# Optimization experiments

Hardware: AMD Instinct MI355X
Metric: run time of the kernel (lower is better)

Reference implementation:

```python
import jax, jax.numpy as jnp
import numpy as np

D, DH, NH = 256, 32, 8  # d_model, d_head, n_heads


def conv2d(x, w, stride=1, padding='VALID', groups=1):
    return jax.lax.conv_general_dilated(
        x, w, (stride, stride), padding,
        feature_group_count=groups,
        dimension_numbers=('NCHW', 'OIHW', 'NCHW'))


def bn2d(x, p):
    # p: [4, C] rows = gamma, beta, running_mean, running_var (inference-mode BN)
    g, b, m, v = p[0], p[1], p[2], p[3]
    inv = g / jnp.sqrt(v + 1e-5)
    return (x - m[:, None, None]) * inv[:, None, None] + b[:, None, None]


def gelu(x):
    return jax.nn.gelu(x, approximate=False)  # torch nn.GELU default (erf)


def to_heads(x):
    # [b, heads*d, h, w] -> [b, h*w, heads, d]
    b, c, h, w = x.shape
    return x.reshape(b, NH, DH, h * w).transpose(0, 3, 1, 2)


def from_heads(x, h, w):
    # [b, h*w, heads, d] -> [b, heads*d, h, w]
    b = x.shape[0]
    return x.transpose(0, 2, 3, 1).reshape(b, NH * DH, h, w)


def linear_attention(q, k, v, eps=1e-6):
    # LoFTR linear attention: phi(x) = elu(x) + 1
    Q = jax.nn.elu(q) + 1.0
    K = jax.nn.elu(k) + 1.0
    L = v.shape[1]
    vn = v / L
    KV = jnp.einsum('nshd,nshv->nhdv', K, vn)
    Z = 1.0 / (jnp.einsum('nlhd,nhd->nlh', Q, K.sum(axis=1)) + eps)
    return jnp.einsum('nlhd,nhdv,nlh->nlhv', Q, KV, Z) * L


def upsample_bilinear_ac(x, s):
    # bilinear, align_corners=True, integer scale factor s (separable H then W)
    def interp(a, axis):
        n_in = a.shape[axis]
        n_out = n_in * s
        pos = jnp.arange(n_out) * ((n_in - 1) / (n_out - 1))
        i0 = jnp.floor(pos).astype(jnp.int32)
        i1 = jnp.minimum(i0 + 1, n_in - 1)
        t = (pos - i0.astype(pos.dtype)).astype(a.dtype)
        sh = [1] * a.ndim
        sh[axis] = n_out
        t = t.reshape(sh)
        return jnp.take(a, i0, axis=axis) * (1 - t) + jnp.take(a, i1, axis=axis) * t
    return interp(interp(x, 2), 3)


def _bn_params(key, c):
    k1, k2, k3, k4 = jax.random.split(key, 4)
    return jnp.stack([
        1.0 + 0.05 * jax.random.normal(k1, (c,)),
        0.05 * jax.random.normal(k2, (c,)),
        0.05 * jax.random.normal(k3, (c,)),
        0.5 + jax.random.uniform(k4, (c,))]).astype(jnp.float32)


def setup_inputs() -> dict:
    key = jax.random.key(0)
    ks = jax.random.split(key, 24)
    B, H, W = 4, 128, 128
    Dm = 4 * D  # MB hidden dim (mlp_ratio=4)

    def w(k, shape, fan_in):
        return (jax.random.normal(k, shape) / np.sqrt(fan_in)).astype(jnp.float32)

    return {
        'x0': jax.random.normal(ks[0], (B, D, H, W), dtype=jnp.float32),
        'scale_weight': jnp.ones((3,), jnp.float32),
        'bn_pre': _bn_params(ks[1], D),
        'wq1': w(ks[2], (D, D, 1, 1), D),
        'wk1': w(ks[3], (D, D, 1, 1), D),
        'wv1': w(ks[4], (D, D, 1, 1), D),
        'wq2': w(ks[5], (D, D, 2, 2), D * 4),
        'wk2': w(ks[6], (D, D, 2, 2), D * 4),
        'wv2': w(ks[7], (D, D, 2, 2), D * 4),
        'wq3': w(ks[8], (D, D, 4, 4), D * 16),
        'wk3': w(ks[9], (D, D, 4, 4), D * 16),
        'wv3': w(ks[10], (D, D, 4, 4), D * 16),
        'merge_w': w(ks[11], (D, D, 1, 1), D),
        'merge_b': 0.01 * jax.random.normal(ks[12], (D,), dtype=jnp.float32),
        'mb_w1': w(ks[13], (Dm, D, 1, 1), D),
        'bn_mb1': _bn_params(ks[14], Dm),
        'mb_wdw': w(ks[15], (Dm, 1, 3, 3), 9),
        'bn_mb2': _bn_params(ks[16], Dm),
        'mb_w2': w(ks[17], (D, Dm, 1, 1), Dm),
        'bn_mb3': _bn_params(ks[18], D),
    }


def reference(x0, scale_weight, bn_pre, wq1, wk1, wv1, wq2, wk2, wv2,
              wq3, wk3, wv3, merge_w, merge_b, mb_w1, bn_mb1, mb_wdw,
              bn_mb2, mb_w2, bn_mb3):
    b, d, h, w = x0.shape
    xn = gelu(bn2d(x0, bn_pre))  # x1 is None -> x1 = x0, shared pre_normact
    # multi-scale conv QKV projections (strides 1, 2, 4)
    q1 = to_heads(conv2d(xn, wq1)); k1 = to_heads(conv2d(xn, wk1)); v1 = to_heads(conv2d(xn, wv1))
    q2 = to_heads(conv2d(xn, wq2, 2)); k2 = to_heads(conv2d(xn, wk2, 2)); v2 = to_heads(conv2d(xn, wv2, 2))
    q3 = to_heads(conv2d(xn, wq3, 4)); k3 = to_heads(conv2d(xn, wk3, 4)); v3 = to_heads(conv2d(xn, wv3, 4))
    o1 = from_heads(linear_attention(q1, k1, v1), h, w)
    o2 = from_heads(linear_attention(q2, k2, v2), h // 2, w // 2)
    o3 = from_heads(linear_attention(q3, k3, v3), h // 4, w // 4)
    o2 = upsample_bilinear_ac(o2, 2)
    o3 = upsample_bilinear_ac(o3, 4)
    sw = jax.nn.softmax(scale_weight)
    message = sw[0] * o1 + sw[1] * o2 + sw[2] * o3
    x = x0 + conv2d(message, merge_w) + merge_b[:, None, None]  # DropPath(0) = id
    # MB mlp: 1x1 expand -> BN -> GELU -> 3x3 depthwise -> BN -> GELU -> 1x1 -> BN
    hm = gelu(bn2d(conv2d(x, mb_w1), bn_mb1))
    hm = gelu(bn2d(conv2d(hm, mb_wdw, 1, ((1, 1), (1, 1)), groups=mb_wdw.shape[0]), bn_mb2))
    mlp_out = bn2d(conv2d(hm, mb_w2), bn_mb3)
    return x + mlp_out
```

## Files before the change

### kernel.cpp

```cpp
#include <hip/hip_runtime.h>
#include <hip/hip_bf16.h>

typedef __attribute__((ext_vector_type(4))) float f32x4;
typedef __attribute__((ext_vector_type(8))) short short8;
typedef unsigned int u32;
typedef unsigned short u16;

__device__ __forceinline__ float bf2f(u16 x) { return __uint_as_float(((u32)x) << 16); }
__device__ __forceinline__ u16 f2bf(float f) {
  u32 u = __float_as_uint(f);
  return (u16)((u + 0x7fffu + ((u >> 16) & 1u)) >> 16);
}
__device__ __forceinline__ float gelu_f(float x) { return 0.5f * x * (1.f + erff(x * 0.7071067811865475f)); }
__device__ __forceinline__ float phi_f(float x) { return x > 0.f ? x + 1.f : __expf(x); }
__device__ __forceinline__ void load8f(const __hip_bfloat16* p, float* f) {
  ushort4 a = *(const ushort4*)p, b = *(const ushort4*)(p + 4);
  f[0] = bf2f(a.x); f[1] = bf2f(a.y); f[2] = bf2f(a.z); f[3] = bf2f(a.w);
  f[4] = bf2f(b.x); f[5] = bf2f(b.y); f[6] = bf2f(b.z); f[7] = bf2f(b.w);
}
__device__ __forceinline__ void cvt8(uint4 u, float* f) {
  f[0] = bf2f((u16)(u.x & 0xffff)); f[1] = bf2f((u16)(u.x >> 16));
  f[2] = bf2f((u16)(u.y & 0xffff)); f[3] = bf2f((u16)(u.y >> 16));
  f[4] = bf2f((u16)(u.z & 0xffff)); f[5] = bf2f((u16)(u.z >> 16));
  f[6] = bf2f((u16)(u.w & 0xffff)); f[7] = bf2f((u16)(u.w >> 16));
}
__device__ __forceinline__ void gload16(const void* g, void* l) {
  __builtin_amdgcn_global_load_lds((const __attribute__((address_space(1))) u32*)g,
                                   (__attribute__((address_space(3))) u32*)l, 16, 0, 0);
}

static constexpr size_t MiB = 1048576ull;
static constexpr size_t OFF_BNP_S = 0, OFF_BNP_T = 1024;
static constexpr size_t OFF_BN1_S = 2048, OFF_BN1_T = 6144;
static constexpr size_t OFF_BN2_S = 10240, OFF_BN2_T = 14336;
static constexpr size_t OFF_BN3_S = 18432, OFF_BN3_T = 19456;
static constexpr size_t OFF_WDW   = 20480;
static constexpr size_t OFF_KV    = 57344;
static constexpr size_t OFF_KSUM  = 450560;
static constexpr size_t OFF_W     = 524288;
static constexpr size_t WF1 = 0;
static constexpr size_t WF2 = 196608;
static constexpr size_t WF3 = 983040;
static constexpr size_t WE_MRG = 4128768;
static constexpr size_t WE_MB1 = 4194304;
static constexpr size_t WE_MB2 = 4456448;
static constexpr size_t OFF_XN    = 20 * MiB;
static constexpr size_t OFF_O1    = 52 * MiB;
static constexpr size_t OFF_O2    = 84 * MiB;
static constexpr size_t OFF_O3    = 92 * MiB;
static constexpr size_t OFF_QKV2  = 96 * MiB;
static constexpr size_t OFF_QKV3  = 120 * MiB;
static constexpr size_t OFF_PART  = 126 * MiB;
static constexpr size_t OFF_QKV1P = 126 * MiB;
static constexpr size_t OFF_MSG   = 126 * MiB;
static constexpr size_t OFF_XB    = 20 * MiB;
static constexpr size_t OFF_HM1   = 52 * MiB;
static constexpr size_t OFF_HM2   = 116 * MiB;
static constexpr size_t WS_NEED   = 180 * MiB;

__global__ __launch_bounds__(256) void fillf(float* p, int n, float v) {
  for (int i = blockIdx.x * 256 + threadIdx.x; i < n; i += gridDim.x * 256) p[i] = v;
}

__global__ __launch_bounds__(256) void bnprep(const float* __restrict__ bn,
                                              float* __restrict__ s, float* __restrict__ t, int C) {
  int c = blockIdx.x * 256 + threadIdx.x;
  if (c >= C) return;
  float g = bn[c], b = bn[C + c], m = bn[2 * C + c], v = bn[3 * C + c];
  float sc = g * rsqrtf(v + 1e-5f);
  s[c] = sc; t[c] = b - m * sc;
}

__global__ __launch_bounds__(256) void wdwprep(const float* __restrict__ w, const float* __restrict__ s,
                                               float* __restrict__ out) {
  int g = blockIdx.x * 256 + threadIdx.x;
  if (g >= 9216) return;
  int c = g & 1023, p = g >> 10;
  out[p * 1024 + c] = w[c * 9 + p] * s[c];
}

__global__ __launch_bounds__(256)
void wprep_all(const float* q1, const float* k1, const float* v1,
               const float* q2, const float* k2, const float* v2,
               const float* q3, const float* k3, const float* v3,
               const float* mrg, const float* m1, const float* m2,
               __hip_bfloat16* __restrict__ pool) {
  int g = blockIdx.x * 256 + threadIdx.x;
  if (g >= 4718592) return;
  const float* src; int C, S; int loc;
  if (g < 196608)      { int seg = g / 65536;   src = seg == 0 ? q1 : seg == 1 ? k1 : v1; C = 256; S = 1; loc = g - seg * 65536; }
  else if (g < 983040) { int r = g - 196608; int seg = r / 262144; src = seg == 0 ? q2 : seg == 1 ? k2 : v2; C = 256; S = 2; loc = r - seg * 262144; }
  else if (g < 4128768){ int r = g - 983040; int seg = r / 1048576; src = seg == 0 ? q3 : seg == 1 ? k3 : v3; C = 256; S = 4; loc = r - seg * 1048576; }
  else if (g < 4194304){ src = mrg; C = 256; S = 1; loc = g - 4128768; }
  else if (g < 4456448){ src = m1; C = 256; S = 1; loc = g - 4194304; }
  else                 { src = m2; C = 1024; S = 1; loc = g - 4456448; }
  int K = C * S * S;
  int o = loc / K, kk = loc - o * K;
  int c = kk % C, p = kk / C;
  pool[g] = __float2bfloat16(src[((size_t)o * C + c) * S * S + p]);
}

__global__ __launch_bounds__(256) void pre_normact(const float* __restrict__ x0, const float* __restrict__ s,
                                                   const float* __restrict__ t, __hip_bfloat16* __restrict__ xn) {
  __shared__ u16 lds[64 * 256];
  const int tid = threadIdx.x;
  const int p0 = blockIdx.x * 64;
  const int b = p0 >> 14, pin = p0 & 16383;
  const float sc = s[tid], sh = t[tid];
  const float* src = x0 + (((size_t)(b * 256 + tid)) << 14) + pin;
  #pragma unroll 4
  for (int j = 0; j < 64; j += 4) {
    float4 v = *(const float4*)(src + j);
    lds[(j + 0) * 256 + tid] = f2bf(gelu_f(v.x * sc + sh));
    lds[(j + 1) * 256 + tid] = f2bf(gelu_f(v.y * sc + sh));
    lds[(j + 2) * 256 + tid] = f2bf(gelu_f(v.z * sc + sh));
    lds[(j + 3) * 256 + tid] = f2bf(gelu_f(v.w * sc + sh));
  }
  __syncthreads();
  const uint4* lsrc = (const uint4*)lds;
  uint4* dst = (uint4*)((u16*)xn + (size_t)p0 * 256);
  #pragma unroll
  for (int i = 0; i < 8; ++i) dst[i * 256 + tid] = lsrc[i * 256 + tid];
}

template <int S, int EPI>
__global__ __launch_bounds__(256)
void gemm_bt(const __hip_bfloat16* __restrict__ A, const __hip_bfloat16* __restrict__ Bw,
             __hip_bfloat16* __restrict__ Cout, int N, int K, int ldb,
             const float* __restrict__ p0, const float* __restrict__ p1,
             const float* __restrict__ xsrc, float* __restrict__ xout, int ksplit) {
  __shared__ __hip_bfloat16 As[2][128 * 64];
  __shared__ __hip_bfloat16 Bs[2][128 * 64];
  const int tid = threadIdx.x;
  const int wave = tid >> 6, lane = tid & 63;
  const int ntn = N >> 7;
  int blk = blockIdx.x;
  { int nwg = gridDim.x; if ((nwg & 7) == 0) { int cpx = nwg >> 3; blk = (blk & 7) * cpx + (blk >> 3); } }
  int kbeg = 0, kend = K;
  float* xo = xout;
  if constexpr (EPI == 7) {
    int tiles = gridDim.x / ksplit;
    int split = blk / tiles; blk -= split * tiles;
    int knum = K / ksplit;
    kbeg = split * knum; kend = kbeg + knum;
    int M = (tiles / ntn) << 7;
    xo = xout + (size_t)split * M * N;
  }
  const int bm = blk / ntn, bnn = blk % ntn;
  const int wr = wave >> 1, wc = wave & 1;
  const int r_lo = lane & 15, r_hi = lane >> 4;
  f32x4 acc[4][4] = {};

  const __hip_bfloat16* aptr[4];
  #pragma unroll
  for (int i = 0; i < 4; ++i) {
    int ci = i * 256 + tid;
    int row = ci >> 3, c8 = ci & 7;
    int m = bm * 128 + row;
    size_t pixbase;
    if constexpr (S == 1) pixbase = (size_t)m * K;
    else if constexpr (S == 2) { int b = m >> 12, y = (m >> 6) & 63, x = m & 63; pixbase = ((size_t)(b * 16384 + y * 256 + x * 2)) * 256; }
    else { int b = m >> 10, y = (m >> 5) & 31, x = m & 31; pixbase = ((size_t)(b * 16384 + y * 512 + x * 4)) * 256; }
    aptr[i] = A + pixbase + c8 * 8;
  }
  const __hip_bfloat16* bptr[4];
  #pragma unroll
  for (int i = 0; i < 4; ++i) {
    int ci = i * 256 + tid;
    int row = ci >> 3, c8 = ci & 7;
    bptr[i] = Bw + (size_t)(bnn * 128 + row) * ldb + c8 * 8;
  }
  const int lofs = wave * 64 * 8;

  auto aoff_of = [&](int k0) -> size_t {
    if constexpr (S == 1) return (size_t)k0;
    else { int pq = k0 >> 8; int dy = pq / S, dx = pq % S; return (size_t)(((dy << 7) + dx) << 8) + (k0 & 255); }
  };

  {
    size_t ao = aoff_of(kbeg);
    #pragma unroll
    for (int i = 0; i < 4; ++i)
      gload16(aptr[i] + ao, (void*)(As[0] + i * 2048 + lofs));
    #pragma unroll
    for (int i = 0; i < 4; ++i)
      gload16(bptr[i] + kbeg, (void*)(Bs[0] + i * 2048 + lofs));
  }
  __syncthreads();

  int cur = 0;
  for (int k0 = kbeg; k0 < kend; k0 += 64) {
    if (k0 + 64 < kend) {
      size_t ao = aoff_of(k0 + 64);
      #pragma unroll
      for (int i = 0; i < 4; ++i)
        gload16(aptr[i] + ao, (void*)(As[cur ^ 1] + i * 2048 + lofs));
      #pragma unroll
      for (int i = 0; i < 4; ++i)
        gload16(bptr[i] + k0 + 64, (void*)(Bs[cur ^ 1] + i * 2048 + lofs));
    }
    const __hip_bfloat16* Ab = As[cur];
    const __hip_bfloat16* Bb = Bs[cur];
    #pragma unroll
    for (int kk = 0; kk < 2; ++kk) {
      short8 af[4], bfr[4];
      #pragma unroll
      for (int mi = 0; mi < 4; ++mi)
        af[mi] = *(const short8*)(Ab + (wr * 64 + mi * 16 + r_lo) * 64 + kk * 32 + r_hi * 8);
      #pragma unroll
      for (int ni = 0; ni < 4; ++ni)
        bfr[ni] = *(const short8*)(Bb + (wc * 64 + ni * 16 + r_lo) * 64 + kk * 32 + r_hi * 8);
      #pragma unroll
      for (int mi = 0; mi < 4; ++mi)
        #pragma unroll
        for (int ni = 0; ni < 4; ++ni)
          acc[mi][ni] = __builtin_amdgcn_mfma_f32_16x16x32_bf16(af[mi], bfr[ni], acc[mi][ni], 0, 0, 0);
    }
    __syncthreads();
    cur ^= 1;
  }

  const int m_base = bm * 128 + wr * 64;
  const int n_base = bnn * 128 + wc * 64;
  #pragma unroll
  for (int mi = 0; mi < 4; ++mi) {
    const int row0 = m_base + mi * 16 + r_hi * 4;
    #pragma unroll
    for (int ni = 0; ni < 4; ++ni) {
      const int col = n_base + ni * 16 + r_lo;
      f32x4 v = acc[mi][ni];
      if constexpr (EPI == 0) {
        #pragma unroll
        for (int j = 0; j < 4; ++j)
          *((u16*)Cout + (size_t)(row0 + j) * N + col) = f2bf(v[j]);
      } else if constexpr (EPI == 1) {
        const float sc = p0[col], sh = p1[col];
        #pragma unroll
        for (int j = 0; j < 4; ++j)
          *((u16*)Cout + (size_t)(row0 + j) * N + col) = f2bf(gelu_f(v[j] * sc + sh));
      } else if constexpr (EPI == 2) {
        const int b = row0 >> 14, pix = row0 & 16383;
        const size_t nchw = (((size_t)(b * 256 + col)) << 14) + pix;
        const float bias = p0[col];
        float4 xv = *(const float4*)(xsrc + nchw);
        float r0 = v[0] + bias + xv.x, r1 = v[1] + bias + xv.y;
        float r2 = v[2] + bias + xv.z, r3 = v[3] + bias + xv.w;
        *(float4*)(xo + nchw) = make_float4(r0, r1, r2, r3);
        *((u16*)Cout + (size_t)(row0 + 0) * 256 + col) = f2bf(r0);
        *((u16*)Cout + (size_t)(row0 + 1) * 256 + col) = f2bf(r1);
        *((u16*)Cout + (size_t)(row0 + 2) * 256 + col) = f2bf(r2);
        *((u16*)Cout + (size_t)(row0 + 3) * 256 + col) = f2bf(r3);
      } else if constexpr (EPI == 7) {
        #pragma unroll
        for (int j = 0; j < 4; ++j)
          xo[(size_t)(row0 + j) * N + col] = v[j];
      } else {
        const int b = row0 >> 14, pix = row0 & 16383;
        const size_t nchw = (((size_t)(b * 256 + col)) << 14) + pix;
        const float sc = p0[col], sh = p1[col];
        float4 pv = *(const float4*)(xo + nchw);
        *(float4*)(xo + nchw) = make_float4(v[0] * sc + sh + pv.x, v[1] * sc + sh + pv.y,
                                            v[2] * sc + sh + pv.z, v[3] * sc + sh + pv.w);
      }
    }
  }
}

__global__ __launch_bounds__(256) void reduce_part(const float* __restrict__ P,
                                                   __hip_bfloat16* __restrict__ out, int MN) {
  int i = (blockIdx.x * 256 + threadIdx.x) * 4;
  if (i >= MN) return;
  float4 a = *(const float4*)(P + i);
  float4 b = *(const float4*)(P + MN + i);
  ushort4 o;
  o.x = f2bf(a.x + b.x); o.y = f2bf(a.y + b.y); o.z = f2bf(a.z + b.z); o.w = f2bf(a.w + b.w);
  *(ushort4*)((u16*)out + i) = o;
}

__global__ __launch_bounds__(256)
void kv_reduce(const __hip_bfloat16* __restrict__ Km, const __hip_bfloat16* __restrict__ Vm,
               float* __restrict__ KV, float* __restrict__ Ksum, int L, int nchunks, int ld) {
  __shared__ float Ks[16][32];
  __shared__ float Vs[16][32];
  const int tid = threadIdx.x;
  const int blk = blockIdx.x;
  const int chunk = blk % nchunks;
  const int bh = blk / nchunks;
  const int h = bh & 7, b = bh >> 3;
  const int d = tid >> 3, v0 = (tid & 7) << 2;
  const int lr = tid >> 4, lq = tid & 15;
  const int cq = (lq & 7) << 2;
  const bool isK = lq < 8;
  const __hip_bfloat16* src = isK ? Km : Vm;
  const int CL = L / nchunks;
  const size_t base = (size_t)(b * L + chunk * CL) * ld + h * 32 + cq;
  float a0 = 0, a1 = 0, a2 = 0, a3 = 0, ks = 0;
  for (int it = 0; it < CL; it += 16) {
    ushort4 u = *(const ushort4*)(src + base + (size_t)(it + lr) * ld);
    float f0 = bf2f(u.x), f1 = bf2f(u.y), f2 = bf2f(u.z), f3 = bf2f(u.w);
    if (isK) {
      Ks[lr][cq + 0] = phi_f(f0); Ks[lr][cq + 1] = phi_f(f1);
      Ks[lr][cq + 2] = phi_f(f2); Ks[lr][cq + 3] = phi_f(f3);
    } else {
      Vs[lr][cq + 0] = f0; Vs[lr][cq + 1] = f1; Vs[lr][cq + 2] = f2; Vs[lr][cq + 3] = f3;
    }
    __syncthreads();
    #pragma unroll
    for (int s = 0; s < 16; ++s) {
      float kk = Ks[s][d];
      ks += kk;
      float4 vv = *(const float4*)&Vs[s][v0];
      a0 += kk * vv.x; a1 += kk * vv.y; a2 += kk * vv.z; a3 += kk * vv.w;
    }
    __syncthreads();
  }
  float* kvp = KV + (size_t)bh * 1024 + d * 32 + v0;
  atomicAdd(kvp + 0, a0); atomicAdd(kvp + 1, a1);
  atomicAdd(kvp + 2, a2); atomicAdd(kvp + 3, a3);
  if ((tid & 7) == 0) atomicAdd(Ksum + bh * 32 + d, ks);
}

__global__ __launch_bounds__(256)
void attn_out(const __hip_bfloat16* __restrict__ Qm, const float* __restrict__ KV,
              const float* __restrict__ Ksum, __hip_bfloat16* __restrict__ O, int lshift, int ld) {
  __shared__ float KVL[8 * 1156];
  __shared__ float KsL[8 * 33];
  const int tid = threadIdx.x;
  const int m0 = blockIdx.x << 5;
  const int bh0 = (m0 >> lshift) << 3;
  #pragma unroll
  for (int i = 0; i < 8; ++i) {
    int id = i * 256 + tid;
    int h = id >> 8, rem = id & 255;
    int d = rem >> 3, vi = rem & 7;
    float4 v = *(const float4*)(KV + (((size_t)(bh0 + h)) << 10) + rem * 4);
    *(float4*)&KVL[h * 1156 + d * 36 + vi * 4] = v;
  }
  { int h = tid >> 5, d = tid & 31; KsL[h * 33 + d] = Ksum[(bh0 + h) * 32 + d]; }
  const int p = tid >> 3, h = tid & 7;
  const u16* qp = (const u16*)Qm + (size_t)(m0 + p) * ld + h * 32;
  float q[32];
  #pragma unroll
  for (int i = 0; i < 4; ++i) {
    uint4 u = *(const uint4*)(qp + i * 8);
    q[i * 8 + 0] = phi_f(bf2f((u16)(u.x & 0xffff))); q[i * 8 + 1] = phi_f(bf2f((u16)(u.x >> 16)));
    q[i * 8 + 2] = phi_f(bf2f((u16)(u.y & 0xffff))); q[i * 8 + 3] = phi_f(bf2f((u16)(u.y >> 16)));
    q[i * 8 + 4] = phi_f(bf2f((u16)(u.z & 0xffff))); q[i * 8 + 5] = phi_f(bf2f((u16)(u.z >> 16)));
    q[i * 8 + 6] = phi_f(bf2f((u16)(u.w & 0xffff))); q[i * 8 + 7] = phi_f(bf2f((u16)(u.w >> 16)));
  }
  __syncthreads();
  const float* kvh = &KVL[h * 1156];
  const float* ksh = &KsL[h * 33];
  float acc[32] = {};
  float z = 0.f;
  #pragma unroll
  for (int d = 0; d < 32; ++d) {
    float qd = q[d];
    z += qd * ksh[d];
    #pragma unroll
    for (int vi = 0; vi < 8; ++vi) {
      float4 kv = *(const float4*)&kvh[d * 36 + vi * 4];
      acc[vi * 4 + 0] += qd * kv.x; acc[vi * 4 + 1] += qd * kv.y;
      acc[vi * 4 + 2] += qd * kv.z; acc[vi * 4 + 3] += qd * kv.w;
    }
  }
  float zi = 1.f / (z + 1e-6f);
  u16* op = (u16*)O + (size_t)(m0 + p) * 256 + h * 32;
  #pragma unroll
  for (int i = 0; i < 4; ++i) {
    uint4 o;
    o.x = (u32)f2bf(acc[i * 8 + 0] * zi) | ((u32)f2bf(acc[i * 8 + 1] * zi) << 16);
    o.y = (u32)f2bf(acc[i * 8 + 2] * zi) | ((u32)f2bf(acc[i * 8 + 3] * zi) << 16);
    o.z = (u32)f2bf(acc[i * 8 + 4] * zi) | ((u32)f2bf(acc[i * 8 + 5] * zi) << 16);
    o.w = (u32)f2bf(acc[i * 8 + 6] * zi) | ((u32)f2bf(acc[i * 8 + 7] * zi) << 16);
    *(uint4*)(op + i * 8) = o;
  }
}

__global__ __launch_bounds__(256)
void message_compose(const __hip_bfloat16* __restrict__ o1, const __hip_bfloat16* __restrict__ o2,
                     const __hip_bfloat16* __restrict__ o3, const float* __restrict__ sw,
                     __hip_bfloat16* __restrict__ msg) {
  const int g = blockIdx.x * 256 + threadIdx.x;
  const int c0 = (g & 31) << 3;
  const int pix = g >> 5;
  const int x = pix & 127, y = (pix >> 7) & 127, b = pix >> 14;
  float w0 = sw[0], w1 = sw[1], w2 = sw[2];
  float mx = fmaxf(w0, fmaxf(w1, w2));
  float e0 = __expf(w0 - mx), e1 = __expf(w1 - mx), e2 = __expf(w2 - mx);
  float inv = 1.f / (e0 + e1 + e2);
  float s0 = e0 * inv, s1 = e1 * inv, s2 = e2 * inv;

  float acc[8], f[8];
  load8f(o1 + (size_t)pix * 256 + c0, f);
  #pragma unroll
  for (int j = 0; j < 8; ++j) acc[j] = s0 * f[j];
  {
    float py = y * (63.f / 127.f); int y0 = (int)py; float ty = py - y0; int y1 = min(y0 + 1, 63);
    float px = x * (63.f / 127.f); int x0 = (int)px; float tx = px - x0; int x1 = min(x0 + 1, 63);
    float wtl = (1 - ty) * (1 - tx), wtr = (1 - ty) * tx, wbl = ty * (1 - tx), wbr = ty * tx;
    const __hip_bfloat16* base = o2 + (size_t)b * 4096 * 256 + c0;
    float f00[8], f01[8], f10[8], f11[8];
    load8f(base + ((size_t)y0 * 64 + x0) * 256, f00);
    load8f(base + ((size_t)y0 * 64 + x1) * 256, f01);
    load8f(base + ((size_t)y1 * 64 + x0) * 256, f10);
    load8f(base + ((size_t)y1 * 64 + x1) * 256, f11);
    #pragma unroll
    for (int j = 0; j < 8; ++j)
      acc[j] += s1 * (wtl * f00[j] + wtr * f01[j] + wbl * f10[j] + wbr * f11[j]);
  }
  {
    float py = y * (31.f / 127.f); int y0 = (int)py; float ty = py - y0; int y1 = min(y0 + 1, 31);
    float px = x * (31.f / 127.f); int x0 = (int)px; float tx = px - x0; int x1 = min(x0 + 1, 31);
    float wtl = (1 - ty) * (1 - tx), wtr = (1 - ty) * tx, wbl = ty * (1 - tx), wbr = ty * tx;
    const __hip_bfloat16* base = o3 + (size_t)b * 1024 * 256 + c0;
    float f00[8], f01[8], f10[8], f11[8];
    load8f(base + ((size_t)y0 * 32 + x0) * 256, f00);
    load8f(base + ((size_t)y0 * 32 + x1) * 256, f01);
    load8f(base + ((size_t)y1 * 32 + x0) * 256, f10);
    load8f(base + ((size_t)y1 * 32 + x1) * 256, f11);
    #pragma unroll
    for (int j = 0; j < 8; ++j)
      acc[j] += s2 * (wtl * f00[j] + wtr * f01[j] + wbl * f10[j] + wbr * f11[j]);
  }
  ushort4 oa, ob;
  oa.x = f2bf(acc[0]); oa.y = f2bf(acc[1]); oa.z = f2bf(acc[2]); oa.w = f2bf(acc[3]);
  ob.x = f2bf(acc[4]); ob.y = f2bf(acc[5]); ob.z = f2bf(acc[6]); ob.w = f2bf(acc[7]);
  *(ushort4*)(msg + (size_t)pix * 256 + c0) = oa;
  *(ushort4*)(msg + (size_t)pix * 256 + c0 + 4) = ob;
}

__global__ __launch_bounds__(256)
void dwconv(const __hip_bfloat16* __restrict__ hm1, const float* __restrict__ wdw,
            const float* __restrict__ t, __hip_bfloat16* __restrict__ hm2) {
  const int g = blockIdx.x * 256 + threadIdx.x;
  const int c0 = (g & 127) << 3;
  const int x = (g >> 7) & 127;
  const int seg = (g >> 14) & 7;
  const int img = g >> 17;
  const int y0 = seg << 4;
  const bool hasL = x > 0, hasR = x < 127;

  float w[9][8];
  #pragma unroll
  for (int t9 = 0; t9 < 9; ++t9) {
    *(float4*)&w[t9][0] = *(const float4*)&wdw[t9 * 1024 + c0];
    *(float4*)&w[t9][4] = *(const float4*)&wdw[t9 * 1024 + c0 + 4];
  }
  float tb[8];
  *(float4*)&tb[0] = *(const float4*)&t[c0];
  *(float4*)&tb[4] = *(const float4*)&t[c0 + 4];

  const __hip_bfloat16* rb = hm1 + (((size_t)(img * 16384 + x)) << 10) + c0;
  __hip_bfloat16* ob = hm2 + (((size_t)(img * 16384 + x)) << 10) + c0;
  const uint4 zz = make_uint4(0, 0, 0, 0);

  float A[8] = {}, B[8] = {};
  for (int r = y0 - 1; r <= y0 + 16; ++r) {
    float l[8], m[8], rv[8];
    uint4 ul = zz, um = zz, ur = zz;
    if ((unsigned)r < 128u) {
      const __hip_bfloat16* pr = rb + ((size_t)r << 17);
      um = *(const uint4*)pr;
      if (hasL) ul = *(const uint4*)(pr - 1024);
      if (hasR) ur = *(const uint4*)(pr + 1024);
    }
    cvt8(ul, l); cvt8(um, m); cvt8(ur, rv);
    if (r > y0) {
      u16 o[8];
      #pragma unroll
      for (int j = 0; j < 8; ++j) {
        float fin = A[j] + w[6][j] * l[j] + w[7][j] * m[j] + w[8][j] * rv[j];
        o[j] = f2bf(gelu_f(fin + tb[j]));
      }
      *(uint4*)(ob + ((size_t)(r - 1) << 17)) = *(uint4*)o;
    }
    if (r < y0 + 16) {
      #pragma unroll
      for (int j = 0; j < 8; ++j) {
        float na = B[j] + w[3][j] * l[j] + w[4][j] * m[j] + w[5][j] * rv[j];
        B[j] = w[0][j] * l[j] + w[1][j] * m[j] + w[2][j] * rv[j];
        A[j] = na;
      }
    }
  }
}

extern "C" void kernel_launch(void* const* d_in, const int* in_sizes, int n_in,
                              void* d_out, int out_size, void* d_ws, size_t ws_size,
                              hipStream_t stream) {
  const float* x0      = (const float*)d_in[0];
  const float* scale_w = (const float*)d_in[1];
  const float* bn_pre  = (const float*)d_in[2];
  const float* wq1 = (const float*)d_in[3];
  const float* wk1 = (const float*)d_in[4];
  const float* wv1 = (const float*)d_in[5];
  const float* wq2 = (const float*)d_in[6];
  const float* wk2 = (const float*)d_in[7];
  const float* wv2 = (const float*)d_in[8];
  const float* wq3 = (const float*)d_in[9];
  const float* wk3 = (const float*)d_in[10];
  const float* wv3 = (const float*)d_in[11];
  const float* merge_w = (const float*)d_in[12];
  const float* merge_b = (const float*)d_in[13];
  const float* mb_w1   = (const float*)d_in[14];
  const float* bn_mb1  = (const float*)d_in[15];
  const float* mb_wdw  = (const float*)d_in[16];
  const float* bn_mb2  = (const float*)d_in[17];
  const float* mb_w2   = (const float*)d_in[18];
  const float* bn_mb3  = (const float*)d_in[19];
  (void)in_sizes; (void)n_in;

  if (ws_size < WS_NEED) {
    fillf<<<4096, 256, 0, stream>>>((float*)d_out, out_size, (float)(ws_size >> 20));
    return;
  }

  char* ws = (char*)d_ws;
  auto F  = [&](size_t off) { return (float*)(ws + off); };
  auto BF = [&](size_t off) { return (__hip_bfloat16*)(ws + off); };
  __hip_bfloat16* Wp = BF(OFF_W);
  float* KV = F(OFF_KV);
  float* KS = F(OFF_KSUM);
  float* Xout = (float*)d_out;

  bnprep<<<1, 256, 0, stream>>>(bn_pre, F(OFF_BNP_S), F(OFF_BNP_T), 256);
  bnprep<<<4, 256, 0, stream>>>(bn_mb1, F(OFF_BN1_S), F(OFF_BN1_T), 1024);
  bnprep<<<4, 256, 0, stream>>>(bn_mb2, F(OFF_BN2_S), F(OFF_BN2_T), 1024);
  bnprep<<<1, 256, 0, stream>>>(bn_mb3, F(OFF_BN3_S), F(OFF_BN3_T), 256);
  wdwprep<<<36, 256, 0, stream>>>(mb_wdw, F(OFF_BN2_S), F(OFF_WDW));
  wprep_all<<<18432, 256, 0, stream>>>(wq1, wk1, wv1, wq2, wk2, wv2, wq3, wk3, wv3,
                                       merge_w, mb_w1, mb_w2, Wp);
  hipMemsetAsync(ws + OFF_KV, 0, 405504, stream);

  pre_normact<<<1024, 256, 0, stream>>>(x0, F(OFF_BNP_S), F(OFF_BNP_T), BF(OFF_XN));

  gemm_bt<2, 0><<<768, 256, 0, stream>>>(BF(OFF_XN), Wp + WF2, BF(OFF_QKV2), 768, 1024, 1024,
                                         nullptr, nullptr, nullptr, nullptr, 1);
  gemm_bt<4, 7><<<384, 256, 0, stream>>>(BF(OFF_XN), Wp + WF3, nullptr, 768, 4096, 4096,
                                         nullptr, nullptr, nullptr, F(OFF_PART), 2);
  reduce_part<<<3072, 256, 0, stream>>>(F(OFF_PART), BF(OFF_QKV3), 4096 * 768);

  kv_reduce<<<256, 256, 0, stream>>>(BF(OFF_QKV2) + 256, BF(OFF_QKV2) + 512, KV + 32768, KS + 1024, 4096, 8, 768);
  kv_reduce<<<256, 256, 0, stream>>>(BF(OFF_QKV3) + 256, BF(OFF_QKV3) + 512, KV + 65536, KS + 2048, 1024, 8, 768);
  attn_out<<<512, 256, 0, stream>>>(BF(OFF_QKV2), KV + 32768, KS + 1024, BF(OFF_O2), 12, 768);
  attn_out<<<128, 256, 0, stream>>>(BF(OFF_QKV3), KV + 65536, KS + 2048, BF(OFF_O3), 10, 768);

  for (int c = 0; c < 2; ++c) {
    const __hip_bfloat16* Ac = BF(OFF_XN) + (size_t)c * 32768 * 256;
    gemm_bt<1, 0><<<1536, 256, 0, stream>>>(Ac, Wp + WF1, BF(OFF_QKV1P), 768, 256, 256,
                                            nullptr, nullptr, nullptr, nullptr, 1);
    kv_reduce<<<512, 256, 0, stream>>>(BF(OFF_QKV1P) + 256, BF(OFF_QKV1P) + 512,
                                       KV + c * 16384, KS + c * 512, 16384, 32, 768);
    attn_out<<<1024, 256, 0, stream>>>(BF(OFF_QKV1P), KV + c * 16384, KS + c * 512,
                                       BF(OFF_O1) + (size_t)c * 32768 * 256, 14, 768);
  }

  message_compose<<<8192, 256, 0, stream>>>(BF(OFF_O1), BF(OFF_O2), BF(OFF_O3), scale_w, BF(OFF_MSG));
  gemm_bt<1, 2><<<1024, 256, 0, stream>>>(BF(OFF_MSG), Wp + WE_MRG, BF(OFF_XB), 256, 256, 256,
                                          merge_b, nullptr, x0, Xout, 1);

  for (int half = 0; half < 2; ++half) {
    const __hip_bfloat16* XBh = BF(OFF_XB) + (size_t)half * 32768 * 256;
    float* Xoh = Xout + (size_t)half * 2 * 256 * 16384;
    gemm_bt<1, 1><<<2048, 256, 0, stream>>>(XBh, Wp + WE_MB1, BF(OFF_HM1), 1024, 256, 256,
                                            F(OFF_BN1_S), F(OFF_BN1_T), nullptr, nullptr, 1);
    dwconv<<<1024, 256, 0, stream>>>(BF(OFF_HM1), F(OFF_WDW), F(OFF_BN2_T), BF(OFF_HM2));
    gemm_bt<1, 8><<<512, 256, 0, stream>>>(BF(OFF_HM2), Wp + WE_MB2, nullptr, 256, 1024, 1024,
                                           F(OFF_BN3_S), F(OFF_BN3_T), nullptr, Xoh, 1);
  }
}
```

Measured before the change: 951.1 us.

## Add 256x256-tile 512-thread GEMM variant and use it for most projections

Adds gemm_bt2, a GEMM kernel with 256x256 output tiles, 8 waves per block and 8x4 MFMA fragments per wave. It replaces the 128x128 kernel for the QKV projections, merge and MB expand GEMMs. The strided-4 projection now splits K four ways and sums with a new four-way reduce. The original kernel is kept only for the final MB projection. The aim is more operand reuse per LDS load and fewer blocks, at the cost of 128 KB shared memory per block, higher register pressure and a larger partial-sum buffer.

```diff
diff --git a/kernel.cpp b/kernel.cpp
--- a/kernel.cpp
+++ b/kernel.cpp
@@ -123,6 +123,18 @@
   for (int i = 0; i < 8; ++i) dst[i * 256 + tid] = lsrc[i * 256 + tid];
 }
 
+template <int S>
+__device__ __forceinline__ size_t pixbase_of(int m, int K) {
+  if constexpr (S == 1) return (size_t)m * K;
+  else if constexpr (S == 2) { int b = m >> 12, y = (m >> 6) & 63, x = m & 63; return ((size_t)(b * 16384 + y * 256 + x * 2)) * 256; }
+  else { int b = m >> 10, y = (m >> 5) & 31, x = m & 31; return ((size_t)(b * 16384 + y * 512 + x * 4)) * 256; }
+}
+template <int S>
+__device__ __forceinline__ size_t aoff_of(int k0) {
+  if constexpr (S == 1) return (size_t)k0;
+  else { int pq = k0 >> 8; int dy = pq / S, dx = pq % S; return (size_t)(((dy << 7) + dx) << 8) + (k0 & 255); }
+}
+
 template <int S, int EPI>
 __global__ __launch_bounds__(256)
 void gemm_bt(const __hip_bfloat16* __restrict__ A, const __hip_bfloat16* __restrict__ Bw,
@@ -136,6 +148,108 @@
   const int ntn = N >> 7;
   int blk = blockIdx.x;
   { int nwg = gridDim.x; if ((nwg & 7) == 0) { int cpx = nwg >> 3; blk = (blk & 7) * cpx + (blk >> 3); } }
+  const int bm = blk / ntn, bnn = blk % ntn;
+  const int wr = wave >> 1, wc = wave & 1;
+  const int r_lo = lane & 15, r_hi = lane >> 4;
+  f32x4 acc[4][4] = {};
+
+  const __hip_bfloat16* aptr[4];
+  #pragma unroll
+  for (int i = 0; i < 4; ++i) {
+    int ci = i * 256 + tid;
+    int row = ci >> 3, c8 = ci & 7;
+    aptr[i] = A + pixbase_of<S>(bm * 128 + row, K) + c8 * 8;
+  }
+  const __hip_bfloat16* bptr[4];
+  #pragma unroll
+  for (int i = 0; i < 4; ++i) {
+    int ci = i * 256 + tid;
+    int row = ci >> 3, c8 = ci & 7;
+    bptr[i] = Bw + (size_t)(bnn * 128 + row) * ldb + c8 * 8;
+  }
+  const int lofs = wave * 512;
+
+  {
+    size_t ao = aoff_of<S>(0);
+    #pragma unroll
+    for (int i = 0; i < 4; ++i)
+      gload16(aptr[i] + ao, (void*)(As[0] + i * 2048 + lofs));
+    #pragma unroll
+    for (int i = 0; i < 4; ++i)
+      gload16(bptr[i], (void*)(Bs[0] + i * 2048 + lofs));
+  }
+  __syncthreads();
+
+  int cur = 0;
+  for (int k0 = 0; k0 < K; k0 += 64) {
+    if (k0 + 64 < K) {
+      size_t ao = aoff_of<S>(k0 + 64);
+      #pragma unroll
+      for (int i = 0; i < 4; ++i)
+        gload16(aptr[i] + ao, (void*)(As[cur ^ 1] + i * 2048 + lofs));
+      #pragma unroll
+      for (int i = 0; i < 4; ++i)
+        gload16(bptr[i] + k0 + 64, (void*)(Bs[cur ^ 1] + i * 2048 + lofs));
+    }
+    const __hip_bfloat16* Ab = As[cur];
+    const __hip_bfloat16* Bb = Bs[cur];
+    #pragma unroll
+    for (int kk = 0; kk < 2; ++kk) {
+      short8 af[4], bfr[4];
+      #pragma unroll
+      for (int mi = 0; mi < 4; ++mi)
+        af[mi] = *(const short8*)(Ab + (wr * 64 + mi * 16 + r_lo) * 64 + kk * 32 + r_hi * 8);
+      #pragma unroll
+      for (int ni = 0; ni < 4; ++ni)
+        bfr[ni] = *(const short8*)(Bb + (wc * 64 + ni * 16 + r_lo) * 64 + kk * 32 + r_hi * 8);
+      #pragma unroll
+      for (int mi = 0; mi < 4; ++mi)
+        #pragma unroll
+        for (int ni = 0; ni < 4; ++ni)
+          acc[mi][ni] = __builtin_amdgcn_mfma_f32_16x16x32_bf16(af[mi], bfr[ni], acc[mi][ni], 0, 0, 0);
+    }
+    __syncthreads();
+    cur ^= 1;
+  }
+
+  const int m_base = bm * 128 + wr * 64;
+  const int n_base = bnn * 128 + wc * 64;
+  #pragma unroll
+  for (int mi = 0; mi < 4; ++mi) {
+    const int row0 = m_base + mi * 16 + r_hi * 4;
+    #pragma unroll
+    for (int ni = 0; ni < 4; ++ni) {
+      const int col = n_base + ni * 16 + r_lo;
+      f32x4 v = acc[mi][ni];
+      if constexpr (EPI == 0) {
+        #pragma unroll
+        for (int j = 0; j < 4; ++j)
+          *((u16*)Cout + (size_t)(row0 + j) * N + col) = f2bf(v[j]);
+      } else {
+        const int b = row0 >> 14, pix = row0 & 16383;
+        const size_t nchw = (((size_t)(b * 256 + col)) << 14) + pix;
+        const float sc = p0[col], sh = p1[col];
+        float4 pv = *(const float4*)(xout + nchw);
+        *(float4*)(xout + nchw) = make_float4(v[0] * sc + sh + pv.x, v[1] * sc + sh + pv.y,
+                                              v[2] * sc + sh + pv.z, v[3] * sc + sh + pv.w);
+      }
+    }
+  }
+}
+
+template <int S, int EPI>
+__global__ __launch_bounds__(512, 2)
+void gemm_bt2(const __hip_bfloat16* __restrict__ A, const __hip_bfloat16* __restrict__ Bw,
+              __hip_bfloat16* __restrict__ Cout, int N, int K, int ldb,
+              const float* __restrict__ p0, const float* __restrict__ p1,
+              const float* __restrict__ xsrc, float* __restrict__ xout, int ksplit) {
+  __shared__ __hip_bfloat16 As[2][256 * 64];
+  __shared__ __hip_bfloat16 Bs[2][256 * 64];
+  const int tid = threadIdx.x;
+  const int wave = tid >> 6, lane = tid & 63;
+  const int ntn = N >> 8;
+  int blk = blockIdx.x;
+  { int nwg = gridDim.x; if ((nwg & 7) == 0) { int cpx = nwg >> 3; blk = (blk & 7) * cpx + (blk >> 3); } }
   int kbeg = 0, kend = K;
   float* xo = xout;
   if constexpr (EPI == 7) {
@@ -143,75 +257,65 @@
     int split = blk / tiles; blk -= split * tiles;
     int knum = K / ksplit;
     kbeg = split * knum; kend = kbeg + knum;
-    int M = (tiles / ntn) << 7;
+    int M = (tiles / ntn) << 8;
     xo = xout + (size_t)split * M * N;
   }
   const int bm = blk / ntn, bnn = blk % ntn;
-  const int wr = wave >> 1, wc = wave & 1;
+  const int wr = wave >> 2, wc = wave & 3;
   const int r_lo = lane & 15, r_hi = lane >> 4;
-  f32x4 acc[4][4] = {};
+  f32x4 acc[8][4] = {};
 
   const __hip_bfloat16* aptr[4];
   #pragma unroll
   for (int i = 0; i < 4; ++i) {
-    int ci = i * 256 + tid;
+    int ci = i * 512 + tid;
     int row = ci >> 3, c8 = ci & 7;
-    int m = bm * 128 + row;
-    size_t pixbase;
-    if constexpr (S == 1) pixbase = (size_t)m * K;
-    else if constexpr (S == 2) { int b = m >> 12, y = (m >> 6) & 63, x = m & 63; pixbase = ((size_t)(b * 16384 + y * 256 + x * 2)) * 256; }
-    else { int b = m >> 10, y = (m >> 5) & 31, x = m & 31; pixbase = ((size_t)(b * 16384 + y * 512 + x * 4)) * 256; }
-    aptr[i] = A + pixbase + c8 * 8;
+    aptr[i] = A + pixbase_of<S>(bm * 256 + row, K) + c8 * 8;
   }
   const __hip_bfloat16* bptr[4];
   #pragma unroll
   for (int i = 0; i < 4; ++i) {
-    int ci = i * 256 + tid;
+    int ci = i * 512 + tid;
     int row = ci >> 3, c8 = ci & 7;
-    bptr[i] = Bw + (size_t)(bnn * 128 + row) * ldb + c8 * 8;
-  }
-  const int lofs = wave * 64 * 8;
-
-  auto aoff_of = [&](int k0) -> size_t {
-    if constexpr (S == 1) return (size_t)k0;
-    else { int pq = k0 >> 8; int dy = pq / S, dx = pq % S; return (size_t)(((dy << 7) + dx) << 8) + (k0 & 255); }
-  };
+    bptr[i] = Bw + (size_t)(bnn * 256 + row) * ldb + c8 * 8;
+  }
+  const int lofs = wave * 512;
 
   {
-    size_t ao = aoff_of(kbeg);
+    size_t ao = aoff_of<S>(kbeg);
     #pragma unroll
     for (int i = 0; i < 4; ++i)
-      gload16(aptr[i] + ao, (void*)(As[0] + i * 2048 + lofs));
+      gload16(aptr[i] + ao, (void*)(As[0] + i * 4096 + lofs));
     #pragma unroll
     for (int i = 0; i < 4; ++i)
-      gload16(bptr[i] + kbeg, (void*)(Bs[0] + i * 2048 + lofs));
+      gload16(bptr[i] + kbeg, (void*)(Bs[0] + i * 4096 + lofs));
   }
   __syncthreads();
 
   int cur = 0;
   for (int k0 = kbeg; k0 < kend; k0 += 64) {
     if (k0 + 64 < kend) {
-      size_t ao = aoff_of(k0 + 64);
+      size_t ao = aoff_of<S>(k0 + 64);
       #pragma unroll
       for (int i = 0; i < 4; ++i)
-        gload16(aptr[i] + ao, (void*)(As[cur ^ 1] + i * 2048 + lofs));
+        gload16(aptr[i] + ao, (void*)(As[cur ^ 1] + i * 4096 + lofs));
       #pragma unroll
       for (int i = 0; i < 4; ++i)
-        gload16(bptr[i] + k0 + 64, (void*)(Bs[cur ^ 1] + i * 2048 + lofs));
+        gload16(bptr[i] + k0 + 64, (void*)(Bs[cur ^ 1] + i * 4096 + lofs));
     }
     const __hip_bfloat16* Ab = As[cur];
     const __hip_bfloat16* Bb = Bs[cur];
     #pragma unroll
     for (int kk = 0; kk < 2; ++kk) {
-      short8 af[4], bfr[4];
-      #pragma unroll
-      for (int mi = 0; mi < 4; ++mi)
-        af[mi] = *(const short8*)(Ab + (wr * 64 + mi * 16 + r_lo) * 64 + kk * 32 + r_hi * 8);
+      short8 af[8], bfr[4];
       #pragma unroll
       for (int ni = 0; ni < 4; ++ni)
         bfr[ni] = *(const short8*)(Bb + (wc * 64 + ni * 16 + r_lo) * 64 + kk * 32 + r_hi * 8);
       #pragma unroll
-      for (int mi = 0; mi < 4; ++mi)
+      for (int mi = 0; mi < 8; ++mi)
+        af[mi] = *(const short8*)(Ab + (wr * 128 + mi * 16 + r_lo) * 64 + kk * 32 + r_hi * 8);
+      #pragma unroll
+      for (int mi = 0; mi < 8; ++mi)
         #pragma unroll
         for (int ni = 0; ni < 4; ++ni)
           acc[mi][ni] = __builtin_amdgcn_mfma_f32_16x16x32_bf16(af[mi], bfr[ni], acc[mi][ni], 0, 0, 0);
@@ -220,10 +324,10 @@
     cur ^= 1;
   }
 
-  const int m_base = bm * 128 + wr * 64;
-  const int n_base = bnn * 128 + wc * 64;
-  #pragma unroll
-  for (int mi = 0; mi < 4; ++mi) {
+  const int m_base = bm * 256 + wr * 128;
+  const int n_base = bnn * 256 + wc * 64;
+  #pragma unroll
+  for (int mi = 0; mi < 8; ++mi) {
     const int row0 = m_base + mi * 16 + r_hi * 4;
     #pragma unroll
     for (int ni = 0; ni < 4; ++ni) {
@@ -250,30 +354,26 @@
         *((u16*)Cout + (size_t)(row0 + 1) * 256 + col) = f2bf(r1);
         *((u16*)Cout + (size_t)(row0 + 2) * 256 + col) = f2bf(r2);
         *((u16*)Cout + (size_t)(row0 + 3) * 256 + col) = f2bf(r3);
-      } else if constexpr (EPI == 7) {
+      } else {
         #pragma unroll
         for (int j = 0; j < 4; ++j)
           xo[(size_t)(row0 + j) * N + col] = v[j];
-      } else {
-        const int b = row0 >> 14, pix = row0 & 16383;
-        const size_t nchw = (((size_t)(b * 256 + col)) << 14) + pix;
-        const float sc = p0[col], sh = p1[col];
-        float4 pv = *(const float4*)(xo + nchw);
-        *(float4*)(xo + nchw) = make_float4(v[0] * sc + sh + pv.x, v[1] * sc + sh + pv.y,
-                                            v[2] * sc + sh + pv.z, v[3] * sc + sh + pv.w);
       }
     }
   }
 }
 
-__global__ __launch_bounds__(256) void reduce_part(const float* __restrict__ P,
-                                                   __hip_bfloat16* __restrict__ out, int MN) {
+__global__ __launch_bounds__(256) void reduce_part4(const float* __restrict__ P,
+                                                    __hip_bfloat16* __restrict__ out, int MN) {
   int i = (blockIdx.x * 256 + threadIdx.x) * 4;
   if (i >= MN) return;
   float4 a = *(const float4*)(P + i);
   float4 b = *(const float4*)(P + MN + i);
+  float4 c = *(const float4*)(P + 2 * (size_t)MN + i);
+  float4 d = *(const float4*)(P + 3 * (size_t)MN + i);
   ushort4 o;
-  o.x = f2bf(a.x + b.x); o.y = f2bf(a.y + b.y); o.z = f2bf(a.z + b.z); o.w = f2bf(a.w + b.w);
+  o.x = f2bf(a.x + b.x + c.x + d.x); o.y = f2bf(a.y + b.y + c.y + d.y);
+  o.z = f2bf(a.z + b.z + c.z + d.z); o.w = f2bf(a.w + b.w + c.w + d.w);
   *(ushort4*)((u16*)out + i) = o;
 }
 
@@ -535,11 +635,11 @@
 
   pre_normact<<<1024, 256, 0, stream>>>(x0, F(OFF_BNP_S), F(OFF_BNP_T), BF(OFF_XN));
 
-  gemm_bt<2, 0><<<768, 256, 0, stream>>>(BF(OFF_XN), Wp + WF2, BF(OFF_QKV2), 768, 1024, 1024,
-                                         nullptr, nullptr, nullptr, nullptr, 1);
-  gemm_bt<4, 7><<<384, 256, 0, stream>>>(BF(OFF_XN), Wp + WF3, nullptr, 768, 4096, 4096,
-                                         nullptr, nullptr, nullptr, F(OFF_PART), 2);
-  reduce_part<<<3072, 256, 0, stream>>>(F(OFF_PART), BF(OFF_QKV3), 4096 * 768);
+  gemm_bt2<2, 0><<<192, 512, 0, stream>>>(BF(OFF_XN), Wp + WF2, BF(OFF_QKV2), 768, 1024, 1024,
+                                          nullptr, nullptr, nullptr, nullptr, 1);
+  gemm_bt2<4, 7><<<192, 512, 0, stream>>>(BF(OFF_XN), Wp + WF3, nullptr, 768, 4096, 4096,
+                                          nullptr, nullptr, nullptr, F(OFF_PART), 4);
+  reduce_part4<<<3072, 256, 0, stream>>>(F(OFF_PART), BF(OFF_QKV3), 4096 * 768);
 
   kv_reduce<<<256, 256, 0, stream>>>(BF(OFF_QKV2) + 256, BF(OFF_QKV2) + 512, KV + 32768, KS + 1024, 4096, 8, 768);
   kv_reduce<<<256, 256, 0, stream>>>(BF(OFF_QKV3) + 256, BF(OFF_QKV3) + 512, KV + 65536, KS + 2048, 1024, 8, 768);
@@ -548,7 +648,7 @@
 
   for (int c = 0; c < 2; ++c) {
     const __hip_bfloat16* Ac = BF(OFF_XN) + (size_t)c * 32768 * 256;
-    gemm_bt<1, 0><<<1536, 256, 0, stream>>>(Ac, Wp + WF1, BF(OFF_QKV1P), 768, 256, 256,
+    gemm_bt2<1, 0><<<384, 512, 0, stream>>>(Ac, Wp + WF1, BF(OFF_QKV1P), 768, 256, 256,
                                             nullptr, nullptr, nullptr, nullptr, 1);
     kv_reduce<<<512, 256, 0, stream>>>(BF(OFF_QKV1P) + 256, BF(OFF_QKV1P) + 512,
                                        KV + c * 16384, KS + c * 512, 16384, 32, 768);
@@ -557,13 +657,13 @@
   }
 
   message_compose<<<8192, 256, 0, stream>>>(BF(OFF_O1), BF(OFF_O2), BF(OFF_O3), scale_w, BF(OFF_MSG));
-  gemm_bt<1, 2><<<1024, 256, 0, stream>>>(BF(OFF_MSG), Wp + WE_MRG, BF(OFF_XB), 256, 256, 256,
+  gemm_bt2<1, 2><<<256, 512, 0, stream>>>(BF(OFF_MSG), Wp + WE_MRG, BF(OFF_XB), 256, 256, 256,
                                           merge_b, nullptr, x0, Xout, 1);
 
   for (int half = 0; half < 2; ++half) {
     const __hip_bfloat16* XBh = BF(OFF_XB) + (size_t)half * 32768 * 256;
     float* Xoh = Xout + (size_t)half * 2 * 256 * 16384;
-    gemm_bt<1, 1><<<2048, 256, 0, stream>>>(XBh, Wp + WE_MB1, BF(OFF_HM1), 1024, 256, 256,
+    gemm_bt2<1, 1><<<512, 512, 0, stream>>>(XBh, Wp + WE_MB1, BF(OFF_HM1), 1024, 256, 256,
                                             F(OFF_BN1_S), F(OFF_BN1_T), nullptr, nullptr, 1);
     dwconv<<<1024, 256, 0, stream>>>(BF(OFF_HM1), F(OFF_WDW), F(OFF_BN2_T), BF(OFF_HM2));
     gemm_bt<1, 8><<<512, 256, 0, stream>>>(BF(OFF_HM2), Wp + WE_MB2, nullptr, 256, 1024, 1024,
```

New measurement: 953.0 us. Within noise of the previous version (+0.2%).
